# Kernel optimization log

Measured on AMD Instinct MI355X. Metric: run time of the kernel, lower is better.

The kernel has to match this reference:

```python
import jax, jax.numpy as jnp
import numpy as np

B, T, D = 4, 2048, 768
E, F, K = 8, 4 * 768, 2


def setup_inputs() -> dict:
    key = jax.random.key(0)
    ks = jax.random.split(key, 5)
    s = 0.02
    return {
        "x": jax.random.normal(ks[0], (B, T, D), dtype=jnp.float32),
        "Wg": jax.random.normal(ks[1], (D, E), dtype=jnp.float32) * s,
        "bg": jnp.zeros((E,), dtype=jnp.float32),
        "W1": jax.random.normal(ks[2], (E, D, F), dtype=jnp.float32) * s,
        "b1": jnp.zeros((E, F), dtype=jnp.float32),
        "W2": jax.random.normal(ks[3], (E, F, D), dtype=jnp.float32) * s,
        "b2": jnp.zeros((E, D), dtype=jnp.float32),
    }


def reference(x, Wg, bg, W1, b1, W2, b2):
    b, t, d = x.shape
    x_flat = x.reshape(-1, d)                      # [N, D]
    n = x_flat.shape[0]

    # Router: softmax over expert logits, take top-2
    gates = jax.nn.softmax(x_flat @ Wg + bg, axis=-1)   # [N, E]
    topk_g, topk_i = jax.lax.top_k(gates, K)            # [N, K]

    # Combine weights: zero for non-selected experts -> math identical to
    # masked dispatch in the torch loop (out = sum_k gate_k * expert_{idx_k}(x))
    combine = jnp.zeros((n, W1.shape[0]), dtype=gates.dtype)
    combine = combine.at[jnp.arange(n)[:, None], topk_i].add(topk_g)  # [N, E]

    # Per-expert MLP applied densely, then weighted combine (zero weights
    # kill non-selected experts' contributions)
    h = jnp.einsum('nd,edf->enf', x_flat, W1) + b1[:, None, :]  # [E, N, F]
    h = jax.nn.gelu(h, approximate=False)                        # torch nn.GELU = exact
    y = jnp.einsum('enf,efd->end', h, W2) + b2[:, None, :]       # [E, N, D]
    out = jnp.einsum('ne,end->nd', combine, y)                   # [N, D]
    return out.reshape(b, t, d)
```

## Files before the change

kernel.cpp:

```cpp
#include <hip/hip_runtime.h>
#include <hip/hip_bf16.h>


#define N_TOK 8192
#define D_DIM 768
#define E_EXP 8
#define F_DIM 3072
#define CAP   8192
#define NT_MAX 136

typedef __attribute__((ext_vector_type(8))) short s8v;
typedef __attribute__((ext_vector_type(4))) float f4v;
typedef unsigned short u16;
typedef unsigned int   u32;
typedef unsigned long long u64;

static __device__ __forceinline__ u16 f2bf(float f) {
    u32 u = __float_as_uint(f);
    return (u16)((u + 0x7fffu + ((u >> 16) & 1u)) >> 16);
}
static __device__ __forceinline__ float gelu_exact(float v) {
    return 0.5f * v * (1.0f + erff(v * 0.70710678118654752440f));
}
static __device__ __forceinline__ void gld_lds16(const u16* g, u16* l) {
    __builtin_amdgcn_global_load_lds(
        (const __attribute__((address_space(1))) void*)g,
        (__attribute__((address_space(3))) void*)l, 16, 0, 0);
}

__global__ __launch_bounds__(256) void moe_gates(
    const float* __restrict__ x, const float* __restrict__ Wg,
    const float* __restrict__ bg, u32* __restrict__ rec_idx,
    float2* __restrict__ rec_g)
{
    const int wave = threadIdx.x >> 6;
    const int lane = threadIdx.x & 63;
    const int t = blockIdx.x * 4 + wave;

    float acc[8];
    #pragma unroll
    for (int e = 0; e < 8; ++e) acc[e] = 0.f;

    const float* xrow = x + (size_t)t * D_DIM + lane * 12;
    #pragma unroll
    for (int i = 0; i < 3; ++i) {
        float4 xv = *(const float4*)(xrow + i * 4);
        float xs[4] = {xv.x, xv.y, xv.z, xv.w};
        #pragma unroll
        for (int j = 0; j < 4; ++j) {
            const int d = lane * 12 + i * 4 + j;
            const float4 w0 = *(const float4*)(Wg + (size_t)d * 8);
            const float4 w1 = *(const float4*)(Wg + (size_t)d * 8 + 4);
            acc[0] += xs[j] * w0.x;  acc[1] += xs[j] * w0.y;
            acc[2] += xs[j] * w0.z;  acc[3] += xs[j] * w0.w;
            acc[4] += xs[j] * w1.x;  acc[5] += xs[j] * w1.y;
            acc[6] += xs[j] * w1.z;  acc[7] += xs[j] * w1.w;
        }
    }
    #pragma unroll
    for (int e = 0; e < 8; ++e) {
        float v = acc[e];
        #pragma unroll
        for (int off = 32; off > 0; off >>= 1) v += __shfl_xor(v, off, 64);
        acc[e] = v + bg[e];
    }
    if (lane == 0) {
        float mx = acc[0];
        #pragma unroll
        for (int e = 1; e < 8; ++e) mx = fmaxf(mx, acc[e]);
        float p[8], s = 0.f;
        #pragma unroll
        for (int e = 0; e < 8; ++e) { p[e] = expf(acc[e] - mx); s += p[e]; }
        const float inv = 1.f / s;
        #pragma unroll
        for (int e = 0; e < 8; ++e) p[e] *= inv;

        int i0 = 0; float g0 = p[0];
        #pragma unroll
        for (int e = 1; e < 8; ++e) if (p[e] > g0) { g0 = p[e]; i0 = e; }
        int i1 = -1; float g1 = -1.f;
        #pragma unroll
        for (int e = 0; e < 8; ++e) if (e != i0 && p[e] > g1) { g1 = p[e]; i1 = e; }

        rec_idx[t] = (u32)i0 | ((u32)i1 << 4);
        rec_g[t] = make_float2(g0, g1);
    }
}

__global__ __launch_bounds__(256) void moe_scatter(
    const u32* __restrict__ rec_idx, const float2* __restrict__ rec_g,
    int* __restrict__ counts, int* __restrict__ tokbuf,
    float* __restrict__ gatebuf)
{
    const int t = blockIdx.x * 256 + threadIdx.x;
    const int lane = threadIdx.x & 63;
    const u32 pk = rec_idx[t];
    const int i0 = pk & 15, i1 = (pk >> 4) & 15;
    const float2 g = rec_g[t];
    const u64 lmask = ((u64)1 << lane) - 1;

    #pragma unroll
    for (int e = 0; e < 8; ++e) {
        const u64 m0 = __ballot(i0 == e);
        const u64 m1 = __ballot(i1 == e);
        const int c0 = __popcll(m0);
        const int total = c0 + __popcll(m1);
        if (total > 0) {
            int base = 0;
            if (lane == 0) base = atomicAdd(&counts[e], total);
            base = __shfl(base, 0, 64);
            if (i0 == e) {
                const int p = base + __popcll(m0 & lmask);
                tokbuf[(size_t)e * CAP + p] = 2 * t;
                gatebuf[(size_t)e * CAP + p] = g.x;
            }
            if (i1 == e) {
                const int p = base + c0 + __popcll(m1 & lmask);
                tokbuf[(size_t)e * CAP + p] = 2 * t + 1;
                gatebuf[(size_t)e * CAP + p] = g.y;
            }
        }
    }
}

__global__ void scan_kernel(const int* __restrict__ counts,
                            int* __restrict__ te, int* __restrict__ tb,
                            int* __restrict__ ntile) {
    if (threadIdx.x == 0) {
        int nt = 0;
        for (int e = 0; e < E_EXP; ++e)
            for (int k = 0; k * 128 < counts[e]; ++k) {
                te[nt] = e; tb[nt] = k * 128; ++nt;
            }
        *ntile = nt;
    }
}

__global__ __launch_bounds__(256) void pack_w(
    const float* __restrict__ src, u16* __restrict__ dst, int K1, int M2)
{
    __shared__ float ls[64][132];
    const int rt = blockIdx.x, kc = blockIdx.y, e = blockIdx.z;
    const int RT = gridDim.x, KC = gridDim.y;
    const float* se = src + (size_t)e * K1 * M2;
    const int tid = threadIdx.x;

    const int kr = tid >> 2, mq = tid & 3;
    const float* srow = se + (size_t)(kc * 64 + kr) * M2 + rt * 128 + mq * 32;
    #pragma unroll
    for (int it = 0; it < 8; ++it)
        *(float4*)&ls[kr][mq * 32 + it * 4] = *(const float4*)(srow + it * 4);
    __syncthreads();

    u16* dt_ = dst + ((size_t)(e * RT + rt) * KC + kc) * 8192;
    const int rr = tid >> 1, hf = tid & 1;
    #pragma unroll
    for (int j = 0; j < 4; ++j) {
        const int c8 = hf * 4 + j;
        union { s8v v; u16 u[8]; } o;
        #pragma unroll
        for (int jj = 0; jj < 8; ++jj) o.u[jj] = f2bf(ls[c8 * 8 + jj][rr]);
        *(s8v*)&dt_[rr * 64 + ((c8 ^ (rr & 7)) * 8)] = o.v;
    }
}

__global__ __launch_bounds__(256) void pack_x(
    const float* __restrict__ x, const int* __restrict__ counts,
    const int* __restrict__ te, const int* __restrict__ tb,
    const int* __restrict__ ntile, const int* __restrict__ tokbuf,
    u16* __restrict__ xg)
{
    const int bx = blockIdx.x, kc = blockIdx.y;
    if (bx >= *ntile) return;
    const int e = te[bx], base = tb[bx], cnt = counts[e];
    const int tid = threadIdx.x;
    const int r = tid >> 1, hf = tid & 1;
    int ent = base + r; if (ent >= cnt) ent = cnt - 1;
    const int tok = tokbuf[(size_t)e * CAP + ent] >> 1;
    const float* xr = x + (size_t)tok * D_DIM + kc * 64 + hf * 32;
    u16* xt = xg + ((size_t)bx * 12 + kc) * 8192 + r * 64;
    #pragma unroll
    for (int j = 0; j < 4; ++j) {
        float4 a = *(const float4*)(xr + j * 8);
        float4 b = *(const float4*)(xr + j * 8 + 4);
        union { s8v v; u16 u[8]; } o;
        o.u[0] = f2bf(a.x); o.u[1] = f2bf(a.y); o.u[2] = f2bf(a.z); o.u[3] = f2bf(a.w);
        o.u[4] = f2bf(b.x); o.u[5] = f2bf(b.y); o.u[6] = f2bf(b.z); o.u[7] = f2bf(b.w);
        *(s8v*)&xt[((hf * 4 + j) ^ (r & 7)) * 8] = o.v;
    }
}

__global__ __launch_bounds__(256) void s1_gemm(
    const u16* __restrict__ xg, const u16* __restrict__ w1g,
    const float* __restrict__ b1, const int* __restrict__ te,
    const int* __restrict__ ntile, u16* __restrict__ hg)
{
    __shared__ u16 Als[8192];
    __shared__ u16 Bls[8192];
    const int bx = blockIdx.x, by = blockIdx.y;
    if (bx >= *ntile) return;
    const int e = te[bx];

    const int tid  = threadIdx.x;
    const int w    = tid >> 6;
    const int lane = tid & 63;
    const int wm   = w & 1, wn = w >> 1;
    const int q    = lane >> 4, ln = lane & 15;

    const u16* Ap = w1g + ((size_t)(e * 24 + by) * 12) * 8192 + w * 2048 + lane * 8;
    const u16* Bp = xg  + ((size_t)bx * 12) * 8192 + w * 2048 + lane * 8;

    f4v acc[4][4];
    #pragma unroll
    for (int mi = 0; mi < 4; ++mi)
        #pragma unroll
        for (int ni = 0; ni < 4; ++ni) acc[mi][ni] = (f4v){0.f,0.f,0.f,0.f};

    for (int s = 0; s < 12; ++s) {
        __syncthreads();
        #pragma unroll
        for (int it = 0; it < 4; ++it) {
            gld_lds16(Ap + it * 512, &Als[w * 2048 + it * 512]);
            gld_lds16(Bp + it * 512, &Bls[w * 2048 + it * 512]);
        }
        Ap += 8192; Bp += 8192;
        __syncthreads();
        #pragma unroll
        for (int kk = 0; kk < 2; ++kk) {
            const int col = ((kk * 4 + q) ^ (ln & 7)) * 8;
            s8v af[4], bf[4];
            #pragma unroll
            for (int mi = 0; mi < 4; ++mi)
                af[mi] = *(const s8v*)&Als[(wm * 64 + mi * 16 + ln) * 64 + col];
            #pragma unroll
            for (int ni = 0; ni < 4; ++ni)
                bf[ni] = *(const s8v*)&Bls[(wn * 64 + ni * 16 + ln) * 64 + col];
            #pragma unroll
            for (int mi = 0; mi < 4; ++mi)
                #pragma unroll
                for (int ni = 0; ni < 4; ++ni)
                    acc[mi][ni] = __builtin_amdgcn_mfma_f32_16x16x32_bf16(
                        af[mi], bf[ni], acc[mi][ni], 0, 0, 0);
        }
    }

    const float* b1e = b1 + (size_t)e * F_DIM + by * 128 + wm * 64;
    u16* ht = hg + ((size_t)bx * 48 + by * 2 + wm) * 8192;
    #pragma unroll
    for (int ni = 0; ni < 4; ++ni) {
        const int rr = wn * 64 + ni * 16 + ln;
        #pragma unroll
        for (int mi = 0; mi < 4; ++mi) {
            const float4 bv = *(const float4*)&b1e[mi * 16 + q * 4];
            u16 us[4];
            us[0] = f2bf(gelu_exact(acc[mi][ni][0] + bv.x));
            us[1] = f2bf(gelu_exact(acc[mi][ni][1] + bv.y));
            us[2] = f2bf(gelu_exact(acc[mi][ni][2] + bv.z));
            us[3] = f2bf(gelu_exact(acc[mi][ni][3] + bv.w));
            uint2 pk;
            pk.x = (u32)us[0] | ((u32)us[1] << 16);
            pk.y = (u32)us[2] | ((u32)us[3] << 16);
            const int c8 = mi * 2 + (q >> 1);
            *(uint2*)&ht[rr * 64 + ((c8 ^ (rr & 7)) * 8) + (q & 1) * 4] = pk;
        }
    }
}

__global__ __launch_bounds__(256) void s2_gemm(
    const u16* __restrict__ hg, const u16* __restrict__ w2g,
    const int* __restrict__ counts, const int* __restrict__ te,
    const int* __restrict__ tb, const int* __restrict__ ntile,
    const int* __restrict__ tokbuf, const float* __restrict__ gatebuf,
    float* __restrict__ y)
{
    __shared__ u16 Als[8192];
    __shared__ u16 Bls[8192];
    __shared__ int   sts[128];
    __shared__ float sg[128];
    const int bx = blockIdx.x, by = blockIdx.y;
    if (bx >= *ntile) return;
    const int e = te[bx], base = tb[bx], cnt = counts[e];

    const int tid  = threadIdx.x;
    const int w    = tid >> 6;
    const int lane = tid & 63;
    const int wm   = w & 1, wn = w >> 1;
    const int q    = lane >> 4, ln = lane & 15;

    if (tid < 128) {
        const int ent = base + tid;
        const bool v = ent < cnt;
        sts[tid] = v ? tokbuf[(size_t)e * CAP + ent] : -1;
        sg[tid]  = v ? gatebuf[(size_t)e * CAP + ent] : 0.f;
    }

    const u16* Ap = w2g + ((size_t)(e * 6 + by) * 48) * 8192 + w * 2048 + lane * 8;
    const u16* Bp = hg  + ((size_t)bx * 48) * 8192 + w * 2048 + lane * 8;

    f4v acc[4][4];
    #pragma unroll
    for (int mi = 0; mi < 4; ++mi)
        #pragma unroll
        for (int ni = 0; ni < 4; ++ni) acc[mi][ni] = (f4v){0.f,0.f,0.f,0.f};

    for (int s = 0; s < 48; ++s) {
        __syncthreads();
        #pragma unroll
        for (int it = 0; it < 4; ++it) {
            gld_lds16(Ap + it * 512, &Als[w * 2048 + it * 512]);
            gld_lds16(Bp + it * 512, &Bls[w * 2048 + it * 512]);
        }
        Ap += 8192; Bp += 8192;
        __syncthreads();
        #pragma unroll
        for (int kk = 0; kk < 2; ++kk) {
            const int col = ((kk * 4 + q) ^ (ln & 7)) * 8;
            s8v af[4], bf[4];
            #pragma unroll
            for (int mi = 0; mi < 4; ++mi)
                af[mi] = *(const s8v*)&Als[(wm * 64 + mi * 16 + ln) * 64 + col];
            #pragma unroll
            for (int ni = 0; ni < 4; ++ni)
                bf[ni] = *(const s8v*)&Bls[(wn * 64 + ni * 16 + ln) * 64 + col];
            #pragma unroll
            for (int mi = 0; mi < 4; ++mi)
                #pragma unroll
                for (int ni = 0; ni < 4; ++ni)
                    acc[mi][ni] = __builtin_amdgcn_mfma_f32_16x16x32_bf16(
                        af[mi], bf[ni], acc[mi][ni], 0, 0, 0);
        }
    }

    #pragma unroll
    for (int ni = 0; ni < 4; ++ni) {
        const int rr = wn * 64 + ni * 16 + ln;
        const int ts = sts[rr];
        if (ts >= 0) {
            const float g = sg[rr];
            float* yr = y + (size_t)ts * D_DIM + by * 128 + wm * 64;
            #pragma unroll
            for (int mi = 0; mi < 4; ++mi) {
                float4 o;
                o.x = g * acc[mi][ni][0];
                o.y = g * acc[mi][ni][1];
                o.z = g * acc[mi][ni][2];
                o.w = g * acc[mi][ni][3];
                *(float4*)&yr[mi * 16 + q * 4] = o;
            }
        }
    }
}

__global__ __launch_bounds__(256) void combine_kernel(
    const float* __restrict__ y, const u32* __restrict__ rec_idx,
    const float2* __restrict__ rec_g, const float* __restrict__ b2,
    float* __restrict__ out)
{
    const int gid = blockIdx.x * 256 + threadIdx.x;
    const int t = gid / 192;
    const int c = (gid - t * 192) * 4;
    const u32 pk = rec_idx[t];
    const int i0 = pk & 15, i1 = (pk >> 4) & 15;
    const float2 g = rec_g[t];
    const float4 a  = *(const float4*)&y[(size_t)(2 * t) * D_DIM + c];
    const float4 b  = *(const float4*)&y[(size_t)(2 * t + 1) * D_DIM + c];
    const float4 ba = *(const float4*)&b2[(size_t)i0 * D_DIM + c];
    const float4 bb = *(const float4*)&b2[(size_t)i1 * D_DIM + c];
    float4 o;
    o.x = g.x * ba.x + g.y * bb.x + a.x + b.x;
    o.y = g.x * ba.y + g.y * bb.y + a.y + b.y;
    o.z = g.x * ba.z + g.y * bb.z + a.z + b.z;
    o.w = g.x * ba.w + g.y * bb.w + a.w + b.w;
    *(float4*)&out[(size_t)t * D_DIM + c] = o;
}

extern "C" void kernel_launch(void* const* d_in, const int* in_sizes, int n_in,
                              void* d_out, int out_size, void* d_ws, size_t ws_size,
                              hipStream_t stream) {
    const float* x  = (const float*)d_in[0];
    const float* Wg = (const float*)d_in[1];
    const float* bg = (const float*)d_in[2];
    const float* W1 = (const float*)d_in[3];
    const float* b1 = (const float*)d_in[4];
    const float* W2 = (const float*)d_in[5];
    const float* b2 = (const float*)d_in[6];
    float* out = (float*)d_out;

    char* ws = (char*)d_ws;
    size_t off = 0;
    u16* xg  = (u16*)(ws + off); off += (size_t)NT_MAX * 12 * 8192 * sizeof(u16);
    u16* w1g = (u16*)(ws + off); off += (size_t)E_EXP * 24 * 12 * 8192 * sizeof(u16);
    u16* w2g = (u16*)(ws + off); off += (size_t)E_EXP * 6 * 48 * 8192 * sizeof(u16);
    u16* hg  = (u16*)(ws + off); off += (size_t)NT_MAX * 48 * 8192 * sizeof(u16);
    float* y = (float*)(ws + off); off += (size_t)2 * N_TOK * D_DIM * sizeof(float);
    int* tokbuf = (int*)(ws + off);      off += (size_t)E_EXP * CAP * sizeof(int);
    float* gatebuf = (float*)(ws + off); off += (size_t)E_EXP * CAP * sizeof(float);
    u32* rec_idx = (u32*)(ws + off);     off += (size_t)N_TOK * sizeof(u32);
    float2* rec_g = (float2*)(ws + off); off += (size_t)N_TOK * sizeof(float2);
    int* counts = (int*)(ws + off);      off += 64;
    int* te     = (int*)(ws + off);      off += NT_MAX * sizeof(int);
    int* tb     = (int*)(ws + off);      off += NT_MAX * sizeof(int);
    int* ntile  = (int*)(ws + off);      off += 64;

    hipMemsetAsync(counts, 0, E_EXP * sizeof(int), stream);

    moe_gates<<<N_TOK / 4, 256, 0, stream>>>(x, Wg, bg, rec_idx, rec_g);
    moe_scatter<<<N_TOK / 256, 256, 0, stream>>>(rec_idx, rec_g, counts, tokbuf, gatebuf);
    scan_kernel<<<1, 64, 0, stream>>>(counts, te, tb, ntile);
    pack_w<<<dim3(24, 12, E_EXP), 256, 0, stream>>>(W1, w1g, D_DIM, F_DIM);
    pack_w<<<dim3(6, 48, E_EXP), 256, 0, stream>>>(W2, w2g, F_DIM, D_DIM);
    pack_x<<<dim3(NT_MAX, 12), 256, 0, stream>>>(x, counts, te, tb, ntile, tokbuf, xg);

    s1_gemm<<<dim3(NT_MAX, 24), 256, 0, stream>>>(xg, w1g, b1, te, ntile, hg);
    s2_gemm<<<dim3(NT_MAX, 6), 256, 0, stream>>>(hg, w2g, counts, te, tb, ntile,
                                                 tokbuf, gatebuf, y);
    combine_kernel<<<(N_TOK * 192) / 256, 256, 0, stream>>>(y, rec_idx, rec_g, b2, out);
}
```

Before: 562.0 us.

## Fuse router and weight packing, widen s1 tile, store expert outputs in bf16

Merges the gating kernel, the counts memset and both weight-packing kernels into one prep kernel to cut launches and let the independent pieces overlap. Doubles the s1 GEMM M-tile to 256 rows, so each x tile is reused across twice as many W1 rows, with launch bounds of 2 blocks per CU. Stores the per-expert outputs y as bf16 instead of fp32, halving that round trip through memory at some precision cost. The larger accumulator array raises register pressure and may lower occupancy.

```diff
diff --git a/kernel.cpp b/kernel.cpp
--- a/kernel.cpp
+++ b/kernel.cpp
@@ -19,6 +19,9 @@
     u32 u = __float_as_uint(f);
     return (u16)((u + 0x7fffu + ((u >> 16) & 1u)) >> 16);
 }
+static __device__ __forceinline__ float bf2f(u16 v) {
+    return __uint_as_float((u32)v << 16);
+}
 static __device__ __forceinline__ float gelu_exact(float v) {
     return 0.5f * v * (1.0f + erff(v * 0.70710678118654752440f));
 }
@@ -28,62 +31,107 @@
         (__attribute__((address_space(3))) void*)l, 16, 0, 0);
 }
 
-__global__ __launch_bounds__(256) void moe_gates(
+__device__ __forceinline__ void pack_w_body(
+    const float* __restrict__ src, u16* __restrict__ dst,
+    int rt, int kc, int e, int K1, int M2, int KC, int TR, int ntm)
+{
+    __shared__ float ls[64][132];
+    const float* se = src + (size_t)e * K1 * M2;
+    const int tid = threadIdx.x;
+
+    const int kr = tid >> 2, mq = tid & 3;
+    const float* srow = se + (size_t)(kc * 64 + kr) * M2 + rt * 128 + mq * 32;
+    #pragma unroll
+    for (int it = 0; it < 8; ++it)
+        *(float4*)&ls[kr][mq * 32 + it * 4] = *(const float4*)(srow + it * 4);
+    __syncthreads();
+
+    u16* dt_ = dst + ((size_t)(e * ntm + (rt * 128) / TR) * KC + kc) * ((size_t)TR * 64)
+                   + (size_t)((rt * 128) % TR) * 64;
+    const int rr = tid >> 1, hf = tid & 1;
+    #pragma unroll
+    for (int j = 0; j < 4; ++j) {
+        const int c8 = hf * 4 + j;
+        union { s8v v; u16 u[8]; } o;
+        #pragma unroll
+        for (int jj = 0; jj < 8; ++jj) o.u[jj] = f2bf(ls[c8 * 8 + jj][rr]);
+        *(s8v*)&dt_[rr * 64 + ((c8 ^ (rr & 7)) * 8)] = o.v;
+    }
+}
+
+__global__ __launch_bounds__(256) void prep_kernel(
     const float* __restrict__ x, const float* __restrict__ Wg,
-    const float* __restrict__ bg, u32* __restrict__ rec_idx,
-    float2* __restrict__ rec_g)
-{
-    const int wave = threadIdx.x >> 6;
-    const int lane = threadIdx.x & 63;
-    const int t = blockIdx.x * 4 + wave;
-
-    float acc[8];
-    #pragma unroll
-    for (int e = 0; e < 8; ++e) acc[e] = 0.f;
-
-    const float* xrow = x + (size_t)t * D_DIM + lane * 12;
-    #pragma unroll
-    for (int i = 0; i < 3; ++i) {
-        float4 xv = *(const float4*)(xrow + i * 4);
-        float xs[4] = {xv.x, xv.y, xv.z, xv.w};
-        #pragma unroll
-        for (int j = 0; j < 4; ++j) {
-            const int d = lane * 12 + i * 4 + j;
-            const float4 w0 = *(const float4*)(Wg + (size_t)d * 8);
-            const float4 w1 = *(const float4*)(Wg + (size_t)d * 8 + 4);
-            acc[0] += xs[j] * w0.x;  acc[1] += xs[j] * w0.y;
-            acc[2] += xs[j] * w0.z;  acc[3] += xs[j] * w0.w;
-            acc[4] += xs[j] * w1.x;  acc[5] += xs[j] * w1.y;
-            acc[6] += xs[j] * w1.z;  acc[7] += xs[j] * w1.w;
-        }
-    }
-    #pragma unroll
-    for (int e = 0; e < 8; ++e) {
-        float v = acc[e];
-        #pragma unroll
-        for (int off = 32; off > 0; off >>= 1) v += __shfl_xor(v, off, 64);
-        acc[e] = v + bg[e];
-    }
-    if (lane == 0) {
-        float mx = acc[0];
-        #pragma unroll
-        for (int e = 1; e < 8; ++e) mx = fmaxf(mx, acc[e]);
-        float p[8], s = 0.f;
-        #pragma unroll
-        for (int e = 0; e < 8; ++e) { p[e] = expf(acc[e] - mx); s += p[e]; }
-        const float inv = 1.f / s;
-        #pragma unroll
-        for (int e = 0; e < 8; ++e) p[e] *= inv;
-
-        int i0 = 0; float g0 = p[0];
-        #pragma unroll
-        for (int e = 1; e < 8; ++e) if (p[e] > g0) { g0 = p[e]; i0 = e; }
-        int i1 = -1; float g1 = -1.f;
-        #pragma unroll
-        for (int e = 0; e < 8; ++e) if (e != i0 && p[e] > g1) { g1 = p[e]; i1 = e; }
-
-        rec_idx[t] = (u32)i0 | ((u32)i1 << 4);
-        rec_g[t] = make_float2(g0, g1);
+    const float* __restrict__ bg, const float* __restrict__ W1,
+    const float* __restrict__ W2, u32* __restrict__ rec_idx,
+    float2* __restrict__ rec_g, u16* __restrict__ w1g,
+    u16* __restrict__ w2g, int* __restrict__ counts)
+{
+    const int bid = blockIdx.x;
+    if (bid == 0 && threadIdx.x < E_EXP) counts[threadIdx.x] = 0;
+
+    if (bid < 2048) {
+        const int wave = threadIdx.x >> 6;
+        const int lane = threadIdx.x & 63;
+        const int t = bid * 4 + wave;
+
+        float acc[8];
+        #pragma unroll
+        for (int e = 0; e < 8; ++e) acc[e] = 0.f;
+
+        const float* xrow = x + (size_t)t * D_DIM + lane * 12;
+        #pragma unroll
+        for (int i = 0; i < 3; ++i) {
+            float4 xv = *(const float4*)(xrow + i * 4);
+            float xs[4] = {xv.x, xv.y, xv.z, xv.w};
+            #pragma unroll
+            for (int j = 0; j < 4; ++j) {
+                const int d = lane * 12 + i * 4 + j;
+                const float4 w0 = *(const float4*)(Wg + (size_t)d * 8);
+                const float4 w1 = *(const float4*)(Wg + (size_t)d * 8 + 4);
+                acc[0] += xs[j] * w0.x;  acc[1] += xs[j] * w0.y;
+                acc[2] += xs[j] * w0.z;  acc[3] += xs[j] * w0.w;
+                acc[4] += xs[j] * w1.x;  acc[5] += xs[j] * w1.y;
+                acc[6] += xs[j] * w1.z;  acc[7] += xs[j] * w1.w;
+            }
+        }
+        #pragma unroll
+        for (int e = 0; e < 8; ++e) {
+            float v = acc[e];
+            #pragma unroll
+            for (int off = 32; off > 0; off >>= 1) v += __shfl_xor(v, off, 64);
+            acc[e] = v + bg[e];
+        }
+        if (lane == 0) {
+            float mx = acc[0];
+            #pragma unroll
+            for (int e = 1; e < 8; ++e) mx = fmaxf(mx, acc[e]);
+            float p[8], s = 0.f;
+            #pragma unroll
+            for (int e = 0; e < 8; ++e) { p[e] = expf(acc[e] - mx); s += p[e]; }
+            const float inv = 1.f / s;
+            #pragma unroll
+            for (int e = 0; e < 8; ++e) p[e] *= inv;
+
+            int i0 = 0; float g0 = p[0];
+            #pragma unroll
+            for (int e = 1; e < 8; ++e) if (p[e] > g0) { g0 = p[e]; i0 = e; }
+            int i1 = -1; float g1 = -1.f;
+            #pragma unroll
+            for (int e = 0; e < 8; ++e) if (e != i0 && p[e] > g1) { g1 = p[e]; i1 = e; }
+
+            rec_idx[t] = (u32)i0 | ((u32)i1 << 4);
+            rec_g[t] = make_float2(g0, g1);
+        }
+    } else if (bid < 4352) {
+        const int id = bid - 2048;
+        const int e = id / 288, rem = id - e * 288;
+        const int rt = rem / 12, kc = rem - rt * 12;
+        pack_w_body(W1, w1g, rt, kc, e, D_DIM, F_DIM, 12, 256, 12);
+    } else {
+        const int id = bid - 4352;
+        const int e = id / 288, rem = id - e * 288;
+        const int rt = rem / 48, kc = rem - rt * 48;
+        pack_w_body(W2, w2g, rt, kc, e, F_DIM, D_DIM, 48, 128, 6);
     }
 }
 
@@ -136,34 +184,6 @@
     }
 }
 
-__global__ __launch_bounds__(256) void pack_w(
-    const float* __restrict__ src, u16* __restrict__ dst, int K1, int M2)
-{
-    __shared__ float ls[64][132];
-    const int rt = blockIdx.x, kc = blockIdx.y, e = blockIdx.z;
-    const int RT = gridDim.x, KC = gridDim.y;
-    const float* se = src + (size_t)e * K1 * M2;
-    const int tid = threadIdx.x;
-
-    const int kr = tid >> 2, mq = tid & 3;
-    const float* srow = se + (size_t)(kc * 64 + kr) * M2 + rt * 128 + mq * 32;
-    #pragma unroll
-    for (int it = 0; it < 8; ++it)
-        *(float4*)&ls[kr][mq * 32 + it * 4] = *(const float4*)(srow + it * 4);
-    __syncthreads();
-
-    u16* dt_ = dst + ((size_t)(e * RT + rt) * KC + kc) * 8192;
-    const int rr = tid >> 1, hf = tid & 1;
-    #pragma unroll
-    for (int j = 0; j < 4; ++j) {
-        const int c8 = hf * 4 + j;
-        union { s8v v; u16 u[8]; } o;
-        #pragma unroll
-        for (int jj = 0; jj < 8; ++jj) o.u[jj] = f2bf(ls[c8 * 8 + jj][rr]);
-        *(s8v*)&dt_[rr * 64 + ((c8 ^ (rr & 7)) * 8)] = o.v;
-    }
-}
-
 __global__ __launch_bounds__(256) void pack_x(
     const float* __restrict__ x, const int* __restrict__ counts,
     const int* __restrict__ te, const int* __restrict__ tb,
@@ -190,12 +210,12 @@
     }
 }
 
-__global__ __launch_bounds__(256) void s1_gemm(
+__global__ __launch_bounds__(256, 2) void s1_gemm(
     const u16* __restrict__ xg, const u16* __restrict__ w1g,
     const float* __restrict__ b1, const int* __restrict__ te,
     const int* __restrict__ ntile, u16* __restrict__ hg)
 {
-    __shared__ u16 Als[8192];
+    __shared__ u16 Als[16384];
     __shared__ u16 Bls[8192];
     const int bx = blockIdx.x, by = blockIdx.y;
     if (bx >= *ntile) return;
@@ -207,36 +227,37 @@
     const int wm   = w & 1, wn = w >> 1;
     const int q    = lane >> 4, ln = lane & 15;
 
-    const u16* Ap = w1g + ((size_t)(e * 24 + by) * 12) * 8192 + w * 2048 + lane * 8;
+    const u16* Ap = w1g + ((size_t)(e * 12 + by) * 12) * 16384 + w * 4096 + lane * 8;
     const u16* Bp = xg  + ((size_t)bx * 12) * 8192 + w * 2048 + lane * 8;
 
-    f4v acc[4][4];
-    #pragma unroll
-    for (int mi = 0; mi < 4; ++mi)
+    f4v acc[8][4];
+    #pragma unroll
+    for (int mi = 0; mi < 8; ++mi)
         #pragma unroll
         for (int ni = 0; ni < 4; ++ni) acc[mi][ni] = (f4v){0.f,0.f,0.f,0.f};
 
     for (int s = 0; s < 12; ++s) {
         __syncthreads();
         #pragma unroll
-        for (int it = 0; it < 4; ++it) {
-            gld_lds16(Ap + it * 512, &Als[w * 2048 + it * 512]);
+        for (int it = 0; it < 8; ++it)
+            gld_lds16(Ap + it * 512, &Als[w * 4096 + it * 512]);
+        #pragma unroll
+        for (int it = 0; it < 4; ++it)
             gld_lds16(Bp + it * 512, &Bls[w * 2048 + it * 512]);
-        }
-        Ap += 8192; Bp += 8192;
+        Ap += 16384; Bp += 8192;
         __syncthreads();
         #pragma unroll
         for (int kk = 0; kk < 2; ++kk) {
             const int col = ((kk * 4 + q) ^ (ln & 7)) * 8;
-            s8v af[4], bf[4];
-            #pragma unroll
-            for (int mi = 0; mi < 4; ++mi)
-                af[mi] = *(const s8v*)&Als[(wm * 64 + mi * 16 + ln) * 64 + col];
+            s8v af[8], bf[4];
+            #pragma unroll
+            for (int mi = 0; mi < 8; ++mi)
+                af[mi] = *(const s8v*)&Als[(wm * 128 + mi * 16 + ln) * 64 + col];
             #pragma unroll
             for (int ni = 0; ni < 4; ++ni)
                 bf[ni] = *(const s8v*)&Bls[(wn * 64 + ni * 16 + ln) * 64 + col];
             #pragma unroll
-            for (int mi = 0; mi < 4; ++mi)
+            for (int mi = 0; mi < 8; ++mi)
                 #pragma unroll
                 for (int ni = 0; ni < 4; ++ni)
                     acc[mi][ni] = __builtin_amdgcn_mfma_f32_16x16x32_bf16(
@@ -244,14 +265,17 @@
         }
     }
 
-    const float* b1e = b1 + (size_t)e * F_DIM + by * 128 + wm * 64;
-    u16* ht = hg + ((size_t)bx * 48 + by * 2 + wm) * 8192;
-    #pragma unroll
-    for (int ni = 0; ni < 4; ++ni) {
-        const int rr = wn * 64 + ni * 16 + ln;
-        #pragma unroll
-        for (int mi = 0; mi < 4; ++mi) {
-            const float4 bv = *(const float4*)&b1e[mi * 16 + q * 4];
+    const float* b1e = b1 + (size_t)e * F_DIM + by * 256;
+    #pragma unroll
+    for (int mi = 0; mi < 8; ++mi) {
+        const int floc = wm * 128 + mi * 16 + q * 4;
+        const int kc   = by * 4 + wm * 2 + (mi >> 2);
+        const int c8   = (mi & 3) * 2 + (q >> 1);
+        const float4 bv = *(const float4*)&b1e[floc];
+        u16* ht = hg + ((size_t)bx * 48 + kc) * 8192;
+        #pragma unroll
+        for (int ni = 0; ni < 4; ++ni) {
+            const int rr = wn * 64 + ni * 16 + ln;
             u16 us[4];
             us[0] = f2bf(gelu_exact(acc[mi][ni][0] + bv.x));
             us[1] = f2bf(gelu_exact(acc[mi][ni][1] + bv.y));
@@ -260,9 +284,10 @@
             uint2 pk;
             pk.x = (u32)us[0] | ((u32)us[1] << 16);
             pk.y = (u32)us[2] | ((u32)us[3] << 16);
-            const int c8 = mi * 2 + (q >> 1);
-            *(uint2*)&ht[rr * 64 + ((c8 ^ (rr & 7)) * 8) + (q & 1) * 4] = pk;
-        }
+            *(uint2*)&hg[((size_t)bx * 48 + kc) * 8192 +
+                         rr * 64 + ((c8 ^ (rr & 7)) * 8) + (q & 1) * 4] = pk;
+        }
+        (void)ht;
     }
 }
 
@@ -271,7 +296,7 @@
     const int* __restrict__ counts, const int* __restrict__ te,
     const int* __restrict__ tb, const int* __restrict__ ntile,
     const int* __restrict__ tokbuf, const float* __restrict__ gatebuf,
-    float* __restrict__ y)
+    u16* __restrict__ y)
 {
     __shared__ u16 Als[8192];
     __shared__ u16 Bls[8192];
@@ -337,22 +362,25 @@
         const int ts = sts[rr];
         if (ts >= 0) {
             const float g = sg[rr];
-            float* yr = y + (size_t)ts * D_DIM + by * 128 + wm * 64;
+            u16* yr = y + (size_t)ts * D_DIM + by * 128 + wm * 64;
             #pragma unroll
             for (int mi = 0; mi < 4; ++mi) {
-                float4 o;
-                o.x = g * acc[mi][ni][0];
-                o.y = g * acc[mi][ni][1];
-                o.z = g * acc[mi][ni][2];
-                o.w = g * acc[mi][ni][3];
-                *(float4*)&yr[mi * 16 + q * 4] = o;
+                u16 us[4];
+                us[0] = f2bf(g * acc[mi][ni][0]);
+                us[1] = f2bf(g * acc[mi][ni][1]);
+                us[2] = f2bf(g * acc[mi][ni][2]);
+                us[3] = f2bf(g * acc[mi][ni][3]);
+                uint2 pk;
+                pk.x = (u32)us[0] | ((u32)us[1] << 16);
+                pk.y = (u32)us[2] | ((u32)us[3] << 16);
+                *(uint2*)&yr[mi * 16 + q * 4] = pk;
             }
         }
     }
 }
 
 __global__ __launch_bounds__(256) void combine_kernel(
-    const float* __restrict__ y, const u32* __restrict__ rec_idx,
+    const u16* __restrict__ y, const u32* __restrict__ rec_idx,
     const float2* __restrict__ rec_g, const float* __restrict__ b2,
     float* __restrict__ out)
 {
@@ -362,15 +390,16 @@
     const u32 pk = rec_idx[t];
     const int i0 = pk & 15, i1 = (pk >> 4) & 15;
     const float2 g = rec_g[t];
-    const float4 a  = *(const float4*)&y[(size_t)(2 * t) * D_DIM + c];
-    const float4 b  = *(const float4*)&y[(size_t)(2 * t + 1) * D_DIM + c];
+    union { uint2 p; u16 u[4]; } a, b;
+    a.p = *(const uint2*)&y[(size_t)(2 * t) * D_DIM + c];
+    b.p = *(const uint2*)&y[(size_t)(2 * t + 1) * D_DIM + c];
     const float4 ba = *(const float4*)&b2[(size_t)i0 * D_DIM + c];
     const float4 bb = *(const float4*)&b2[(size_t)i1 * D_DIM + c];
     float4 o;
-    o.x = g.x * ba.x + g.y * bb.x + a.x + b.x;
-    o.y = g.x * ba.y + g.y * bb.y + a.y + b.y;
-    o.z = g.x * ba.z + g.y * bb.z + a.z + b.z;
-    o.w = g.x * ba.w + g.y * bb.w + a.w + b.w;
+    o.x = g.x * ba.x + g.y * bb.x + bf2f(a.u[0]) + bf2f(b.u[0]);
+    o.y = g.x * ba.y + g.y * bb.y + bf2f(a.u[1]) + bf2f(b.u[1]);
+    o.z = g.x * ba.z + g.y * bb.z + bf2f(a.u[2]) + bf2f(b.u[2]);
+    o.w = g.x * ba.w + g.y * bb.w + bf2f(a.u[3]) + bf2f(b.u[3]);
     *(float4*)&out[(size_t)t * D_DIM + c] = o;
 }
 
@@ -389,10 +418,10 @@
     char* ws = (char*)d_ws;
     size_t off = 0;
     u16* xg  = (u16*)(ws + off); off += (size_t)NT_MAX * 12 * 8192 * sizeof(u16);
-    u16* w1g = (u16*)(ws + off); off += (size_t)E_EXP * 24 * 12 * 8192 * sizeof(u16);
-    u16* w2g = (u16*)(ws + off); off += (size_t)E_EXP * 6 * 48 * 8192 * sizeof(u16);
+    u16* w1g = (u16*)(ws + off); off += (size_t)E_EXP * F_DIM * D_DIM * sizeof(u16);
+    u16* w2g = (u16*)(ws + off); off += (size_t)E_EXP * D_DIM * F_DIM * sizeof(u16);
     u16* hg  = (u16*)(ws + off); off += (size_t)NT_MAX * 48 * 8192 * sizeof(u16);
-    float* y = (float*)(ws + off); off += (size_t)2 * N_TOK * D_DIM * sizeof(float);
+    u16* y   = (u16*)(ws + off); off += (size_t)2 * N_TOK * D_DIM * sizeof(u16);
     int* tokbuf = (int*)(ws + off);      off += (size_t)E_EXP * CAP * sizeof(int);
     float* gatebuf = (float*)(ws + off); off += (size_t)E_EXP * CAP * sizeof(float);
     u32* rec_idx = (u32*)(ws + off);     off += (size_t)N_TOK * sizeof(u32);
@@ -402,16 +431,13 @@
     int* tb     = (int*)(ws + off);      off += NT_MAX * sizeof(int);
     int* ntile  = (int*)(ws + off);      off += 64;
 
-    hipMemsetAsync(counts, 0, E_EXP * sizeof(int), stream);
-
-    moe_gates<<<N_TOK / 4, 256, 0, stream>>>(x, Wg, bg, rec_idx, rec_g);
+    prep_kernel<<<6656, 256, 0, stream>>>(x, Wg, bg, W1, W2, rec_idx, rec_g,
+                                          w1g, w2g, counts);
     moe_scatter<<<N_TOK / 256, 256, 0, stream>>>(rec_idx, rec_g, counts, tokbuf, gatebuf);
     scan_kernel<<<1, 64, 0, stream>>>(counts, te, tb, ntile);
-    pack_w<<<dim3(24, 12, E_EXP), 256, 0, stream>>>(W1, w1g, D_DIM, F_DIM);
-    pack_w<<<dim3(6, 48, E_EXP), 256, 0, stream>>>(W2, w2g, F_DIM, D_DIM);
     pack_x<<<dim3(NT_MAX, 12), 256, 0, stream>>>(x, counts, te, tb, ntile, tokbuf, xg);
 
-    s1_gemm<<<dim3(NT_MAX, 24), 256, 0, stream>>>(xg, w1g, b1, te, ntile, hg);
+    s1_gemm<<<dim3(NT_MAX, 12), 256, 0, stream>>>(xg, w1g, b1, te, ntile, hg);
     s2_gemm<<<dim3(NT_MAX, 6), 256, 0, stream>>>(hg, w2g, counts, te, tb, ntile,
                                                  tokbuf, gatebuf, y);
     combine_kernel<<<(N_TOK * 192) / 256, 256, 0, stream>>>(y, rec_idx, rec_g, b2, out);
```

Measured after the change: 537.1 us. 1.05x faster.
